# Kernel tuning notes

Hardware: AMD Instinct MI355X
Metric: run time of the kernel (lower is better)

The kernel has to match this reference:

```python
import jax, jax.numpy as jnp
import numpy as np

N = 100000
E = 1600000
F_IN = 64
F_OUT = 64
C = 1.0
MIN_NORM = 1e-15
BALL_EPS = 4e-3  # float32 eps in HGCN PoincareBall.proj


def _norm(x):
    return jnp.clip(jnp.linalg.norm(x, axis=-1, keepdims=True), MIN_NORM)


def artanh(x):
    return jnp.arctanh(jnp.clip(x, -1.0 + 1e-7, 1.0 - 1e-7))


def proj(x, c):
    # project back onto the Poincare ball of curvature -c
    norm = _norm(x)
    maxnorm = (1.0 - BALL_EPS) / jnp.sqrt(c)
    return jnp.where(norm > maxnorm, x / norm * maxnorm, x)


def mobius_matvec(m, x, c):
    sqrt_c = jnp.sqrt(c)
    x_norm = _norm(x)
    mx = x @ m.T
    mx_norm = _norm(mx)
    res = jnp.tanh(mx_norm / x_norm * artanh(sqrt_c * x_norm)) * mx / (mx_norm * sqrt_c)
    zero_mx = jnp.all(mx == 0, axis=-1, keepdims=True)
    return jnp.where(zero_mx, jnp.zeros_like(res), res)


def expmap0(u, c):
    sqrt_c = jnp.sqrt(c)
    u_norm = _norm(u)
    return jnp.tanh(sqrt_c * u_norm) * u / (sqrt_c * u_norm)


def mobius_add(x, y, c):
    x2 = jnp.sum(x * x, axis=-1, keepdims=True)
    y2 = jnp.sum(y * y, axis=-1, keepdims=True)
    xy = jnp.sum(x * y, axis=-1, keepdims=True)
    num = (1.0 + 2.0 * c * xy + c * y2) * x + (1.0 - c * x2) * y
    denom = 1.0 + 2.0 * c * xy + c * c * x2 * y2
    return num / jnp.clip(denom, MIN_NORM)


def hyp_linear(x, W, b, c):
    res = proj(mobius_matvec(W, x, c), c)
    if b is not None:
        hyp_bias = proj(expmap0(b[None, :], c), c)
        res = proj(mobius_add(res, hyp_bias, c), c)
    return res


def scatter_mean(edge_index, x, n):
    # mean of source features over edges landing at each target node; 0 if isolated
    src, dst = edge_index[0], edge_index[1]
    s = jax.ops.segment_sum(x[src], dst, num_segments=n)
    cnt = jax.ops.segment_sum(jnp.ones((src.shape[0], 1), x.dtype), dst, num_segments=n)
    return s / jnp.clip(cnt, 1.0)


def setup_inputs() -> dict:
    key = jax.random.key(0)
    ks = jax.random.split(key, 9)
    glorot = 1.0 / np.sqrt(F_IN)
    return {
        "x": jax.random.normal(ks[0], (N, F_IN), dtype=jnp.float32) * 0.1,
        "W_pos": jax.random.uniform(ks[1], (F_OUT, F_IN), jnp.float32, -glorot, glorot),
        "W_pos_cc": jax.random.uniform(ks[2], (F_OUT, F_IN), jnp.float32, -glorot, glorot),
        "b_pos_cc": jax.random.uniform(ks[3], (F_OUT,), jnp.float32, -glorot, glorot),
        "W_neg": jax.random.uniform(ks[4], (F_OUT, F_IN), jnp.float32, -glorot, glorot),
        "W_neg_cc": jax.random.uniform(ks[5], (F_OUT, F_IN), jnp.float32, -glorot, glorot),
        "b_neg_cc": jax.random.uniform(ks[6], (F_OUT,), jnp.float32, -glorot, glorot),
        "pos_edge_index": jax.random.randint(ks[7], (2, E), 0, N, dtype=jnp.int64) if jax.config.jax_enable_x64 else jax.random.randint(ks[7], (2, E), 0, N, dtype=jnp.int32),
        "neg_edge_index": jax.random.randint(ks[8], (2, E), 0, N, dtype=jnp.int32),
    }


def reference(x, W_pos, W_pos_cc, b_pos_cc, W_neg, W_neg_cc, b_neg_cc, pos_edge_index, neg_edge_index):
    n = x.shape[0]
    # first_aggr=True branch of HSignedConv.forward
    agg_pos = scatter_mean(pos_edge_index, x, n)          # [N, F_IN]
    out_pos = hyp_linear(agg_pos, W_pos, None, C)
    out_pos = out_pos + hyp_linear(x, W_pos_cc, b_pos_cc, C)
    agg_neg = scatter_mean(neg_edge_index, x, n)
    out_neg = hyp_linear(agg_neg, W_neg, None, C)
    out_neg = out_neg + hyp_linear(x, W_neg_cc, b_neg_cc, C)
    return jnp.concatenate([out_pos, out_neg], axis=-1)  # [N, 2*F_OUT]
```

## Files before the change

kernel.cpp:

```cpp
#include <hip/hip_runtime.h>
#include <math.h>

#define NN 100000
#define BSZ 256
#define NB 391
#define NB2 782
#define RBSLOTS 50048
constexpr float MAXNORM_C = 0.996f;
constexpr float MINNORM_C = 1e-15f;

__global__ void prep_transpose(const float* __restrict__ Wp, const float* __restrict__ Wpc,
                               const float* __restrict__ Wn, const float* __restrict__ Wnc,
                               float* __restrict__ wt) {
    int idx = blockIdx.x * 256 + threadIdx.x;
    int m = idx >> 12;
    int k = (idx >> 6) & 63;
    int j = idx & 63;
    const float* W = (m == 0) ? Wp : (m == 1) ? Wpc : (m == 2) ? Wn : Wnc;
    wt[idx] = W[j * 64 + k];
}

__device__ inline float wave_sum64(float v) {
    #pragma unroll
    for (int m = 32; m >= 1; m >>= 1) v += __shfl_xor(v, m, 64);
    return v;
}

__global__ void prep_bias(const float* __restrict__ bp, const float* __restrict__ bn,
                          float* __restrict__ hb) {
    int l = threadIdx.x;
    #pragma unroll
    for (int h = 0; h < 2; ++h) {
        float u = (h ? bn : bp)[l];
        float norm = fmaxf(sqrtf(wave_sum64(u * u)), MINNORM_C);
        float s = tanhf(norm) / norm;
        float v = s * u;
        float vn = fmaxf(sqrtf(wave_sum64(v * v)), MINNORM_C);
        if (vn > MAXNORM_C) v *= MAXNORM_C / vn;
        float y2 = wave_sum64(v * v);
        hb[h * 65 + l] = v;
        if (l == 0) hb[h * 65 + 64] = y2;
    }
}

__global__ __launch_bounds__(256) void bucket_count(
    const int* __restrict__ pei, int E1,
    const int* __restrict__ nei, int E2,
    int* __restrict__ gcnt) {
    __shared__ int h[NB2];
    int tid = threadIdx.x;
    for (int i = tid; i < NB2; i += 256) h[i] = 0;
    __syncthreads();
    int tot = E1 + E2;
    int base = blockIdx.x * 8192;
    #pragma unroll 4
    for (int k = 0; k < 32; ++k) {
        int idx = base + k * 256 + tid;
        if (idx < tot) {
            int half = idx >= E1;
            int e = idx - (half ? E1 : 0);
            const int* ei = half ? nei : pei;
            int E = half ? E2 : E1;
            int dst = ei[E + e];
            atomicAdd(&h[half * NB + (dst >> 8)], 1);
        }
    }
    __syncthreads();
    for (int i = tid; i < NB2; i += 256) {
        int c = h[i];
        if (c) atomicAdd(&gcnt[i], c);
    }
}

__global__ void bucket_scan(const int* __restrict__ gcnt, int* __restrict__ goffs,
                            int* __restrict__ gcursor) {
    __shared__ int tmp[256];
    int tid = threadIdx.x;
    int base = tid * 4;
    int items[4];
    int s = 0;
    #pragma unroll
    for (int i = 0; i < 4; ++i) {
        items[i] = (base + i < NB2) ? gcnt[base + i] : 0;
        s += items[i];
    }
    tmp[tid] = s;
    __syncthreads();
    for (int off = 1; off < 256; off <<= 1) {
        int v = (tid >= off) ? tmp[tid - off] : 0;
        __syncthreads();
        tmp[tid] += v;
        __syncthreads();
    }
    int run = tmp[tid] - s;
    #pragma unroll
    for (int i = 0; i < 4; ++i) {
        if (base + i < NB2) { goffs[base + i] = run; gcursor[base + i] = run; }
        run += items[i];
    }
}

__global__ __launch_bounds__(256) void bucket_scatter(
    const int* __restrict__ pei, int E1,
    const int* __restrict__ nei, int E2,
    int* __restrict__ gcursor, int* __restrict__ packed) {
    __shared__ int h[NB2];
    __shared__ int hb[NB2];
    int tid = threadIdx.x;
    for (int i = tid; i < NB2; i += 256) h[i] = 0;
    __syncthreads();
    int tot = E1 + E2;
    int base = blockIdx.x * 8192;
    #pragma unroll 4
    for (int k = 0; k < 32; ++k) {
        int idx = base + k * 256 + tid;
        if (idx < tot) {
            int half = idx >= E1;
            int e = idx - (half ? E1 : 0);
            const int* ei = half ? nei : pei;
            int E = half ? E2 : E1;
            int dst = ei[E + e];
            atomicAdd(&h[half * NB + (dst >> 8)], 1);
        }
    }
    __syncthreads();
    for (int i = tid; i < NB2; i += 256) {
        int c = h[i];
        hb[i] = c ? atomicAdd(&gcursor[i], c) : 0;
    }
    __syncthreads();
    for (int i = tid; i < NB2; i += 256) h[i] = 0;
    __syncthreads();
    #pragma unroll 4
    for (int k = 0; k < 32; ++k) {
        int idx = base + k * 256 + tid;
        if (idx < tot) {
            int half = idx >= E1;
            int e = idx - (half ? E1 : 0);
            const int* ei = half ? nei : pei;
            int E = half ? E2 : E1;
            int src = ei[e];
            int dst = ei[E + e];
            int b = half * NB + (dst >> 8);
            int r = atomicAdd(&h[b], 1);
            packed[hb[b] + r] = (src << 8) | (dst & 255);
        }
    }
}

__global__ __launch_bounds__(256) void node_sort(
    const int* __restrict__ goffs, const int* __restrict__ gcnt,
    const int* __restrict__ packed,
    int* __restrict__ esrc, int* __restrict__ ndeg, int* __restrict__ noffs) {
    __shared__ int h[256];
    __shared__ int sc[256];
    int tid = threadIdx.x;
    int bucket = blockIdx.x;
    int start = goffs[bucket];
    int cnt = gcnt[bucket];
    h[tid] = 0;
    __syncthreads();
    for (int i = start + tid; i < start + cnt; i += 256)
        atomicAdd(&h[packed[i] & 255], 1);
    __syncthreads();
    int deg = h[tid];
    sc[tid] = deg;
    __syncthreads();
    for (int off = 1; off < 256; off <<= 1) {
        int v = (tid >= off) ? sc[tid - off] : 0;
        __syncthreads();
        sc[tid] += v;
        __syncthreads();
    }
    int excl = sc[tid] - deg;
    int half = bucket >= NB;
    int node = (bucket - (half ? NB : 0)) * BSZ + tid;
    if (node < NN) {
        ndeg[half * NN + node] = deg;
        noffs[half * NN + node] = start + excl;
    }
    h[tid] = excl;
    __syncthreads();
    for (int i = start + tid; i < start + cnt; i += 256) {
        int p = packed[i];
        int r = atomicAdd(&h[p & 255], 1);
        esrc[start + r] = p >> 8;
    }
}

__global__ __launch_bounds__(256) void gather_kernel(
    const int* __restrict__ noffs, const int* __restrict__ ndeg,
    const int* __restrict__ esrc, const float* __restrict__ x,
    float* __restrict__ out) {
    int wid = (blockIdx.x * 256 + threadIdx.x) >> 6;
    int lane = threadIdx.x & 63;
    if (wid >= 2 * NN) return;
    int half = wid >= NN;
    int node = wid - (half ? NN : 0);
    int start = noffs[wid];
    int deg = ndeg[wid];
    float acc = 0.f;
    for (int b = 0; b < deg; b += 64) {
        int n = min(64, deg - b);
        int s_l = (b + lane < deg) ? esrc[start + b + lane] : 0;
        int i = 0;
        for (; i + 4 <= n; i += 4) {
            int a0 = __shfl(s_l, i, 64), a1 = __shfl(s_l, i + 1, 64);
            int a2 = __shfl(s_l, i + 2, 64), a3 = __shfl(s_l, i + 3, 64);
            float v0 = x[a0 * 64 + lane], v1 = x[a1 * 64 + lane];
            float v2 = x[a2 * 64 + lane], v3 = x[a3 * 64 + lane];
            acc += (v0 + v1) + (v2 + v3);
        }
        for (; i < n; ++i) acc += x[__shfl(s_l, i, 64) * 64 + lane];
    }
    float m = acc / fmaxf((float)deg, 1.f);
    out[(size_t)node * 128 + half * 64 + lane] = m;
}

__device__ __attribute__((always_inline)) inline void mm1_lds(
        const float* p, const float4* wl, float (&m)[64], float& vn2out) {
    #pragma unroll
    for (int j = 0; j < 64; ++j) m[j] = 0.f;
    float vn2 = 0.f;
    #pragma unroll 1
    for (int k0 = 0; k0 < 64; k0 += 4) {
        float4 a = *(const float4*)(p + k0);
        vn2 = fmaf(a.x, a.x, fmaf(a.y, a.y, fmaf(a.z, a.z, fmaf(a.w, a.w, vn2))));
        const float4* wk = wl + k0 * 16;
        #pragma unroll
        for (int j4 = 0; j4 < 16; ++j4) {
            float4 w0 = wk[j4];
            float4 w1 = wk[16 + j4];
            float4 w2 = wk[32 + j4];
            float4 w3 = wk[48 + j4];
            int j = j4 * 4;
            m[j+0] = fmaf(a.x,w0.x, fmaf(a.y,w1.x, fmaf(a.z,w2.x, fmaf(a.w,w3.x, m[j+0]))));
            m[j+1] = fmaf(a.x,w0.y, fmaf(a.y,w1.y, fmaf(a.z,w2.y, fmaf(a.w,w3.y, m[j+1]))));
            m[j+2] = fmaf(a.x,w0.z, fmaf(a.y,w1.z, fmaf(a.z,w2.z, fmaf(a.w,w3.z, m[j+2]))));
            m[j+3] = fmaf(a.x,w0.w, fmaf(a.y,w1.w, fmaf(a.z,w2.w, fmaf(a.w,w3.w, m[j+3]))));
        }
    }
    vn2out = vn2;
}

__device__ __attribute__((always_inline)) inline void mm1_s(
        const float* p, const float* __restrict__ wtm, float (&m)[64], float& vn2out) {
    #pragma unroll
    for (int j = 0; j < 64; ++j) m[j] = 0.f;
    float vn2 = 0.f;
    for (int k0 = 0; k0 < 64; k0 += 4) {
        float4 a = *(const float4*)(p + k0);
        vn2 = fmaf(a.x, a.x, fmaf(a.y, a.y, fmaf(a.z, a.z, fmaf(a.w, a.w, vn2))));
        const float* w0 = wtm + k0 * 64;
        #pragma unroll
        for (int j = 0; j < 64; ++j) {
            float mm = m[j];
            mm = fmaf(a.x, w0[j],        mm);
            mm = fmaf(a.y, w0[64 + j],   mm);
            mm = fmaf(a.z, w0[128 + j],  mm);
            mm = fmaf(a.w, w0[192 + j],  mm);
            m[j] = mm;
        }
    }
    vn2out = vn2;
}

__device__ __attribute__((always_inline)) inline void mob_scale_proj(
        float (&m)[64], float vn2) {
    float mn2 = 0.f;
    #pragma unroll
    for (int j = 0; j < 64; ++j) mn2 = fmaf(m[j], m[j], mn2);
    float xnorm = fmaxf(sqrtf(vn2), MINNORM_C);
    float mnorm = fmaxf(sqrtf(mn2), MINNORM_C);
    float z = fminf(xnorm, 1.0f - 1e-7f);
    float art = 0.5f * logf((1.0f + z) / (1.0f - z));
    float t = tanhf(mnorm / xnorm * art);
    float scale = (mn2 == 0.f) ? 0.f : (t / mnorm);
    #pragma unroll
    for (int j = 0; j < 64; ++j) m[j] *= scale;
    float rn2 = 0.f;
    #pragma unroll
    for (int j = 0; j < 64; ++j) rn2 = fmaf(m[j], m[j], rn2);
    float rnorm = fmaxf(sqrtf(rn2), MINNORM_C);
    float f = (rnorm > MAXNORM_C) ? (MAXNORM_C / rnorm) : 1.0f;
    #pragma unroll
    for (int j = 0; j < 64; ++j) m[j] *= f;
}

__device__ __attribute__((always_inline)) inline float bias_addf(
        float (&m)[64], const float* hbv) {
    float x2 = 0.f, xy = 0.f;
    #pragma unroll
    for (int j = 0; j < 64; ++j) {
        float h = hbv[j];
        x2 = fmaf(m[j], m[j], x2);
        xy = fmaf(m[j], h, xy);
    }
    float y2 = hbv[64];
    float A = 1.f + 2.f * xy + y2;
    float Bc = 1.f - x2;
    float den = 1.f + 2.f * xy + x2 * y2;
    float dinv = 1.f / fmaxf(den, MINNORM_C);
    float rn2 = 0.f;
    #pragma unroll
    for (int j = 0; j < 64; ++j) {
        float r = (A * m[j] + Bc * hbv[j]) * dinv;
        m[j] = r;
        rn2 = fmaf(r, r, rn2);
    }
    float rnorm = fmaxf(sqrtf(rn2), MINNORM_C);
    return (rnorm > MAXNORM_C) ? (MAXNORM_C / rnorm) : 1.0f;
}

__global__ __launch_bounds__(256, 2) void finalize_kernel(
    const float* __restrict__ x,
    const float* __restrict__ wt,
    const float* __restrict__ hb,
    float* __restrict__ rb,
    float* __restrict__ out) {
    __shared__ float4 wlds[1024];
    __shared__ __align__(16) float hbs[68];
    int tid = threadIdx.x;
    int half = blockIdx.x & 1;

    const float4* wsrc = (const float4*)(wt + half * 8192);
    #pragma unroll
    for (int i = 0; i < 4; ++i) wlds[i * 256 + tid] = wsrc[i * 256 + tid];
    if (tid < 65) hbs[tid] = hb[half * 65 + tid];
    __syncthreads();

    int node = (blockIdx.x >> 1) * 256 + tid;
    bool valid = node < NN;
    int nc = valid ? node : NN - 1;
    float* op = out + (size_t)nc * 128 + half * 64;
    const float* wtb = wt + half * 8192 + 4096;

    if (tid < 128) {
        {
            float m[64]; float vn2;
            mm1_lds(op, wlds, m, vn2);
            mob_scale_proj(m, vn2);
            if (valid) {
                #pragma unroll
                for (int k0 = 0; k0 < 64; k0 += 4)
                    *(float4*)(op + k0) = make_float4(m[k0], m[k0+1], m[k0+2], m[k0+3]);
            }
        }
        {
            float m[64]; float vn2;
            mm1_s(x + (size_t)nc * 64, wtb, m, vn2);
            mob_scale_proj(m, vn2);
            float f = bias_addf(m, hbs);
            if (valid) {
                #pragma unroll
                for (int k0 = 0; k0 < 64; k0 += 4) {
                    float4 a = *(const float4*)(op + k0);
                    a.x += m[k0 + 0] * f;
                    a.y += m[k0 + 1] * f;
                    a.z += m[k0 + 2] * f;
                    a.w += m[k0 + 3] * f;
                    *(float4*)(op + k0) = a;
                }
            }
        }
    } else {
        float* rp = rb + ((size_t)half * RBSLOTS + (size_t)(blockIdx.x >> 1) * 128
                          + (tid - 128)) * 64;
        {
            float m[64]; float vn2;
            mm1_s(x + (size_t)nc * 64, wtb, m, vn2);
            mob_scale_proj(m, vn2);
            float f = bias_addf(m, hbs);
            if (valid) {
                #pragma unroll
                for (int k0 = 0; k0 < 64; k0 += 4)
                    *(float4*)(rp + k0) = make_float4(m[k0]*f, m[k0+1]*f,
                                                      m[k0+2]*f, m[k0+3]*f);
            }
        }
        {
            float m[64]; float vn2;
            mm1_lds(op, wlds, m, vn2);
            mob_scale_proj(m, vn2);
            if (valid) {
                #pragma unroll
                for (int k0 = 0; k0 < 64; k0 += 4) {
                    float4 b = *(const float4*)(rp + k0);
                    *(float4*)(op + k0) = make_float4(m[k0+0] + b.x, m[k0+1] + b.y,
                                                      m[k0+2] + b.z, m[k0+3] + b.w);
                }
            }
        }
    }
}

extern "C" void kernel_launch(void* const* d_in, const int* in_sizes, int n_in,
                              void* d_out, int out_size, void* d_ws, size_t ws_size,
                              hipStream_t stream) {
    const float* x   = (const float*)d_in[0];
    const float* Wp  = (const float*)d_in[1];
    const float* Wpc = (const float*)d_in[2];
    const float* bp  = (const float*)d_in[3];
    const float* Wn  = (const float*)d_in[4];
    const float* Wnc = (const float*)d_in[5];
    const float* bn  = (const float*)d_in[6];
    const int* pei = (const int*)d_in[7];
    const int* nei = (const int*)d_in[8];
    float* out = (float*)d_out;

    int E1 = in_sizes[7] / 2;
    int E2 = in_sizes[8] / 2;
    int tot = E1 + E2;

    int*   gcnt    = (int*)d_ws;
    int*   goffs   = gcnt + NB2;
    int*   gcursor = goffs + NB2;
    int*   ndeg    = gcursor + NB2 + 2;
    int*   noffs   = ndeg + 2 * NN;
    float* hbp     = (float*)(noffs + 2 * NN);
    float* wt      = hbp + 192;
    int*   packed  = (int*)(wt + 16384);
    int*   esrc    = packed + tot;
    float* rb      = (float*)packed;

    hipMemsetAsync(gcnt, 0, NB2 * sizeof(int), stream);

    prep_transpose<<<64, 256, 0, stream>>>(Wp, Wpc, Wn, Wnc, wt);
    prep_bias<<<1, 64, 0, stream>>>(bp, bn, hbp);

    int nblk = (tot + 8191) / 8192;
    bucket_count<<<nblk, 256, 0, stream>>>(pei, E1, nei, E2, gcnt);
    bucket_scan<<<1, 256, 0, stream>>>(gcnt, goffs, gcursor);
    bucket_scatter<<<nblk, 256, 0, stream>>>(pei, E1, nei, E2, gcursor, packed);
    node_sort<<<NB2, 256, 0, stream>>>(goffs, gcnt, packed, esrc, ndeg, noffs);

    gather_kernel<<<(2 * NN * 64 + 255) / 256, 256, 0, stream>>>(noffs, ndeg, esrc, x, out);

    int fblocks = 2 * ((NN + 255) / 256);
    finalize_kernel<<<fblocks, 256, 0, stream>>>(x, wt, hbp, rb, out);
}
```

Baseline: 423.3 us.

## Fuse node sort and gather into per-bucket LDS atomic accumulation

Shrinks the destination buckets from 256 to 128 nodes and replaces the node_sort plus per-node gather kernels with a single bucket_gather kernel. Each 512-thread block streams its bucket's packed edges, gathers source rows of x and accumulates them into a 32KB shared-memory tile with LDS float atomics, counting degrees the same way. This removes the esrc/ndeg/noffs arrays, one full pass over the edge list, and a kernel launch. In exchange it relies on LDS float atomicAdd throughput, whose contention pattern depends on the degree distribution, gives lower occupancy from the larger shared tile, and makes float summation order nondeterministic.

```diff
diff --git a/kernel.cpp b/kernel.cpp
--- a/kernel.cpp
+++ b/kernel.cpp
@@ -2,9 +2,9 @@
 #include <math.h>
 
 #define NN 100000
-#define BSZ 256
-#define NB 391
-#define NB2 782
+#define GSZ 128
+#define NB 782
+#define NB2 1564
 #define RBSLOTS 50048
 constexpr float MAXNORM_C = 0.996f;
 constexpr float MINNORM_C = 1e-15f;
@@ -62,7 +62,7 @@
             const int* ei = half ? nei : pei;
             int E = half ? E2 : E1;
             int dst = ei[E + e];
-            atomicAdd(&h[half * NB + (dst >> 8)], 1);
+            atomicAdd(&h[half * NB + (dst >> 7)], 1);
         }
     }
     __syncthreads();
@@ -76,11 +76,11 @@
                             int* __restrict__ gcursor) {
     __shared__ int tmp[256];
     int tid = threadIdx.x;
-    int base = tid * 4;
-    int items[4];
+    int base = tid * 8;
+    int items[8];
     int s = 0;
     #pragma unroll
-    for (int i = 0; i < 4; ++i) {
+    for (int i = 0; i < 8; ++i) {
         items[i] = (base + i < NB2) ? gcnt[base + i] : 0;
         s += items[i];
     }
@@ -94,7 +94,7 @@
     }
     int run = tmp[tid] - s;
     #pragma unroll
-    for (int i = 0; i < 4; ++i) {
+    for (int i = 0; i < 8; ++i) {
         if (base + i < NB2) { goffs[base + i] = run; gcursor[base + i] = run; }
         run += items[i];
     }
@@ -120,7 +120,7 @@
             const int* ei = half ? nei : pei;
             int E = half ? E2 : E1;
             int dst = ei[E + e];
-            atomicAdd(&h[half * NB + (dst >> 8)], 1);
+            atomicAdd(&h[half * NB + (dst >> 7)], 1);
         }
     }
     __syncthreads();
@@ -141,80 +141,70 @@
             int E = half ? E2 : E1;
             int src = ei[e];
             int dst = ei[E + e];
-            int b = half * NB + (dst >> 8);
+            int b = half * NB + (dst >> 7);
             int r = atomicAdd(&h[b], 1);
-            packed[hb[b] + r] = (src << 8) | (dst & 255);
-        }
-    }
-}
-
-__global__ __launch_bounds__(256) void node_sort(
+            packed[hb[b] + r] = (src << 7) | (dst & 127);
+        }
+    }
+}
+
+__global__ __launch_bounds__(512) void bucket_gather(
     const int* __restrict__ goffs, const int* __restrict__ gcnt,
-    const int* __restrict__ packed,
-    int* __restrict__ esrc, int* __restrict__ ndeg, int* __restrict__ noffs) {
-    __shared__ int h[256];
-    __shared__ int sc[256];
+    const int* __restrict__ packed, const float* __restrict__ x,
+    float* __restrict__ out) {
+    __shared__ __align__(16) float acc[GSZ * 64];
+    __shared__ int deg[GSZ];
     int tid = threadIdx.x;
     int bucket = blockIdx.x;
+    int half = bucket >= NB;
+    int b = bucket - (half ? NB : 0);
     int start = goffs[bucket];
     int cnt = gcnt[bucket];
-    h[tid] = 0;
-    __syncthreads();
-    for (int i = start + tid; i < start + cnt; i += 256)
-        atomicAdd(&h[packed[i] & 255], 1);
-    __syncthreads();
-    int deg = h[tid];
-    sc[tid] = deg;
-    __syncthreads();
-    for (int off = 1; off < 256; off <<= 1) {
-        int v = (tid >= off) ? sc[tid - off] : 0;
-        __syncthreads();
-        sc[tid] += v;
-        __syncthreads();
-    }
-    int excl = sc[tid] - deg;
-    int half = bucket >= NB;
-    int node = (bucket - (half ? NB : 0)) * BSZ + tid;
-    if (node < NN) {
-        ndeg[half * NN + node] = deg;
-        noffs[half * NN + node] = start + excl;
-    }
-    h[tid] = excl;
-    __syncthreads();
-    for (int i = start + tid; i < start + cnt; i += 256) {
-        int p = packed[i];
-        int r = atomicAdd(&h[p & 255], 1);
-        esrc[start + r] = p >> 8;
-    }
-}
-
-__global__ __launch_bounds__(256) void gather_kernel(
-    const int* __restrict__ noffs, const int* __restrict__ ndeg,
-    const int* __restrict__ esrc, const float* __restrict__ x,
-    float* __restrict__ out) {
-    int wid = (blockIdx.x * 256 + threadIdx.x) >> 6;
-    int lane = threadIdx.x & 63;
-    if (wid >= 2 * NN) return;
-    int half = wid >= NN;
-    int node = wid - (half ? NN : 0);
-    int start = noffs[wid];
-    int deg = ndeg[wid];
-    float acc = 0.f;
-    for (int b = 0; b < deg; b += 64) {
-        int n = min(64, deg - b);
-        int s_l = (b + lane < deg) ? esrc[start + b + lane] : 0;
+    #pragma unroll
+    for (int i = 0; i < 16; ++i) acc[i * 512 + tid] = 0.f;
+    if (tid < GSZ) deg[tid] = 0;
+    __syncthreads();
+
+    int lane = tid & 63;
+    int end = start + cnt;
+    for (int base0 = start + (tid >> 6) * 64; base0 < end; base0 += 512) {
+        int n = min(64, end - base0);
+        int p_l = (base0 + lane < end) ? packed[base0 + lane] : 0;
+        if (lane < n) atomicAdd(&deg[p_l & 127], 1);
         int i = 0;
         for (; i + 4 <= n; i += 4) {
-            int a0 = __shfl(s_l, i, 64), a1 = __shfl(s_l, i + 1, 64);
-            int a2 = __shfl(s_l, i + 2, 64), a3 = __shfl(s_l, i + 3, 64);
-            float v0 = x[a0 * 64 + lane], v1 = x[a1 * 64 + lane];
-            float v2 = x[a2 * 64 + lane], v3 = x[a3 * 64 + lane];
-            acc += (v0 + v1) + (v2 + v3);
-        }
-        for (; i < n; ++i) acc += x[__shfl(s_l, i, 64) * 64 + lane];
-    }
-    float m = acc / fmaxf((float)deg, 1.f);
-    out[(size_t)node * 128 + half * 64 + lane] = m;
+            int p0 = __shfl(p_l, i, 64), p1 = __shfl(p_l, i + 1, 64);
+            int p2 = __shfl(p_l, i + 2, 64), p3 = __shfl(p_l, i + 3, 64);
+            float v0 = x[(p0 >> 7) * 64 + lane];
+            float v1 = x[(p1 >> 7) * 64 + lane];
+            float v2 = x[(p2 >> 7) * 64 + lane];
+            float v3 = x[(p3 >> 7) * 64 + lane];
+            atomicAdd(&acc[(p0 & 127) * 64 + lane], v0);
+            atomicAdd(&acc[(p1 & 127) * 64 + lane], v1);
+            atomicAdd(&acc[(p2 & 127) * 64 + lane], v2);
+            atomicAdd(&acc[(p3 & 127) * 64 + lane], v3);
+        }
+        for (; i < n; ++i) {
+            int p = __shfl(p_l, i, 64);
+            atomicAdd(&acc[(p & 127) * 64 + lane], x[(p >> 7) * 64 + lane]);
+        }
+    }
+    __syncthreads();
+
+    int nodebase = b * GSZ;
+    #pragma unroll
+    for (int k = 0; k < 4; ++k) {
+        int idx4 = k * 512 + tid;
+        int nl = idx4 >> 4;
+        int f0 = (idx4 & 15) * 4;
+        int gnode = nodebase + nl;
+        if (gnode < NN) {
+            float d = fmaxf((float)deg[nl], 1.f);
+            float4 v = *(const float4*)&acc[nl * 64 + f0];
+            *(float4*)&out[(size_t)gnode * 128 + half * 64 + f0] =
+                make_float4(v.x / d, v.y / d, v.z / d, v.w / d);
+        }
+    }
 }
 
 __device__ __attribute__((always_inline)) inline void mm1_lds(
@@ -415,12 +405,9 @@
     int*   gcnt    = (int*)d_ws;
     int*   goffs   = gcnt + NB2;
     int*   gcursor = goffs + NB2;
-    int*   ndeg    = gcursor + NB2 + 2;
-    int*   noffs   = ndeg + 2 * NN;
-    float* hbp     = (float*)(noffs + 2 * NN);
+    float* hbp     = (float*)(gcursor + NB2 + 2);
     float* wt      = hbp + 192;
     int*   packed  = (int*)(wt + 16384);
-    int*   esrc    = packed + tot;
     float* rb      = (float*)packed;
 
     hipMemsetAsync(gcnt, 0, NB2 * sizeof(int), stream);
@@ -432,9 +419,8 @@
     bucket_count<<<nblk, 256, 0, stream>>>(pei, E1, nei, E2, gcnt);
     bucket_scan<<<1, 256, 0, stream>>>(gcnt, goffs, gcursor);
     bucket_scatter<<<nblk, 256, 0, stream>>>(pei, E1, nei, E2, gcursor, packed);
-    node_sort<<<NB2, 256, 0, stream>>>(goffs, gcnt, packed, esrc, ndeg, noffs);
-
-    gather_kernel<<<(2 * NN * 64 + 255) / 256, 256, 0, stream>>>(noffs, ndeg, esrc, x, out);
+
+    bucket_gather<<<NB2, 512, 0, stream>>>(goffs, gcnt, packed, x, out);
 
     int fblocks = 2 * ((NN + 255) / 256);
     finalize_kernel<<<fblocks, 256, 0, stream>>>(x, wt, hbp, rb, out);
```

Measured after the change: 1.481 ms. 3.5x slower.
